# Optimization experiments

Measured on AMD Instinct MI355X. Metric: run time of the kernel, lower is better.

Reference implementation:

```python
import jax, jax.numpy as jnp
import numpy as np

PATCH = 16
H_RES, W_RES = 512, 512
PREFIX = 8
NUM_HEADS = 12
DIM = 768
GAUSS_STD = 5.0


def gauss_addition():
    # n_patches = (w//16, h//16); addition[(i,j),(k,l)] = exp(-((i-k)^2+(j-l)^2)/(2*std^2))
    d1, d2 = W_RES // PATCH, H_RES // PATCH  # (32, 32)
    inv2s2 = 1.0 / (2.0 * GAUSS_STD * GAUSS_STD)
    i = jnp.arange(d1, dtype=jnp.float32)
    j = jnp.arange(d2, dtype=jnp.float32)
    Ai = jnp.exp(-((i[:, None] - i[None, :]) ** 2) * inv2s2)  # [d1,d1]
    Aj = jnp.exp(-((j[:, None] - j[None, :]) ** 2) * inv2s2)  # [d2,d2]
    add = jnp.einsum('ik,jl->ijkl', Ai, Aj).reshape(d1 * d2, d1 * d2)
    # zero rows/cols for the prefix tokens (prepended)
    return jnp.pad(add, ((PREFIX, 0), (PREFIX, 0)))  # [N,N]


def setup_inputs() -> dict:
    key = jax.random.key(0)
    ks = jax.random.split(key, 5)
    N = (W_RES // PATCH) * (H_RES // PATCH) + PREFIX  # 1032
    B, C = 8, DIM
    x = jax.random.normal(ks[0], (B, N, C), dtype=jnp.float32)
    w_qkv = jax.random.normal(ks[1], (3 * C, C), dtype=jnp.float32) * 0.02
    b_qkv = jax.random.normal(ks[2], (3 * C,), dtype=jnp.float32) * 0.02
    w_proj = jax.random.normal(ks[3], (C, C), dtype=jnp.float32) * 0.02
    b_proj = jax.random.normal(ks[4], (C,), dtype=jnp.float32) * 0.02
    return {'x': x, 'w_qkv': w_qkv, 'b_qkv': b_qkv, 'w_proj': w_proj, 'b_proj': b_proj}


def reference(x, w_qkv, b_qkv, w_proj, b_proj):
    B, N, C = x.shape
    H = NUM_HEADS
    hd = C // H
    scale = hd ** -0.5
    qkv = x @ w_qkv.T + b_qkv              # [B,N,3C]
    k = qkv[..., C:2 * C].reshape(B, N, H, hd)
    v = qkv[..., 2 * C:].reshape(B, N, H, hd)
    add = gauss_addition().astype(x.dtype)  # [N,N], broadcast over B,H
    scores = jnp.einsum('bnhd,bmhd->bhnm', k, k) * scale + add
    attn = jax.nn.softmax(scores, axis=-1)
    out = jnp.einsum('bhnm,bmhd->bnhd', attn, v).reshape(B, N, C)
    return out @ w_proj.T + b_proj
```

## Files before the change

### kernel.cpp

```cpp
#include <hip/hip_runtime.h>
#include <hip/hip_bf16.h>

typedef unsigned short u16;
typedef __bf16 bf16x8 __attribute__((ext_vector_type(8)));
typedef __bf16 bf16x4 __attribute__((ext_vector_type(4)));
typedef float f32x4 __attribute__((ext_vector_type(4)));

#define DEVI __device__ __forceinline__

#if __has_builtin(__builtin_amdgcn_exp2f)
#define EXP2 __builtin_amdgcn_exp2f
#else
#define EXP2 exp2f
#endif

constexpr int Bn = 8, Nn = 1032, Cn = 768, Hn = 12, HDn = 64;
constexpr int NQPc = 1088;
constexpr int NVM = 1088;
constexpr int MTOT = Bn * Nn;
constexpr int MPAD = 8320;
constexpr int KVN = 1536;
constexpr int PFXc = 8;
constexpr int NPADQ = NVM - Nn;
constexpr float SCALEc = 0.125f;
constexpr float LOG2Ec = 1.4426950408889634f;
constexpr float C1c = SCALEc * LOG2Ec;
constexpr float INV2S2c = 0.02f;
constexpr float K2c = INV2S2c * LOG2Ec;

constexpr size_t OFF_XB  = 0;
constexpr size_t SZ_XB   = (size_t)MPAD * Cn * 2;
constexpr size_t OFF_AT  = OFF_XB;
constexpr size_t OFF_WKV = OFF_XB + SZ_XB;
constexpr size_t SZ_WKV  = (size_t)KVN * Cn * 2;
constexpr size_t OFF_WP  = OFF_WKV + SZ_WKV;
constexpr size_t SZ_WP   = (size_t)Cn * Cn * 2;
constexpr size_t OFF_K   = OFF_WP + SZ_WP;
constexpr size_t SZ_K    = (size_t)Bn * Hn * NQPc * HDn * 2;
constexpr size_t OFF_V   = OFF_K + SZ_K;
constexpr size_t SZ_V    = (size_t)Bn * Hn * HDn * NVM * 2;

DEVI u16 f2bf(float f) {
  __bf16 h = (__bf16)f;
  return *reinterpret_cast<u16*>(&h);
}

DEVI void glds16(const void* g, void* l) {
  __builtin_amdgcn_global_load_lds((const __attribute__((address_space(1))) void*)g,
                                   (__attribute__((address_space(3))) void*)l, 16, 0, 0);
}

__global__ __launch_bounds__(256) void prep_kernel(
    const float* __restrict__ x, const float* __restrict__ wqkv,
    const float* __restrict__ wproj, u16* __restrict__ xb,
    u16* __restrict__ wkvb, u16* __restrict__ wpb,
    u16* __restrict__ khead, u16* __restrict__ vT) {
  const int n1 = MPAD * Cn / 4, n2 = KVN * Cn / 4, n3 = Cn * Cn / 4;
  const int z1 = 96 * 448;
  const int z2 = 6144 * 7;
  const int nc = n1 + n2 + n3;
  const int tot = nc + z1 + z2;
  for (int i = blockIdx.x * blockDim.x + threadIdx.x; i < tot; i += gridDim.x * blockDim.x) {
    if (i < nc) {
      const float* src; u16* dst;
      if (i < n1) {
        int e = i * 4;
        src = (e < MTOT * Cn) ? (x + e) : nullptr;
        dst = xb + e;
      } else if (i < n1 + n2) {
        int e = (i - n1) * 4;
        src = wqkv + Cn * Cn + e;
        dst = wkvb + e;
      } else {
        int e = (i - n1 - n2) * 4;
        src = wproj + e;
        dst = wpb + e;
      }
      float4 f = src ? *(const float4*)src : make_float4(0.f, 0.f, 0.f, 0.f);
      *(ushort4*)dst = make_ushort4(f2bf(f.x), f2bf(f.y), f2bf(f.z), f2bf(f.w));
    } else if (i < nc + z1) {
      int j = i - nc, bh = j / 448, c = j - bh * 448;
      char* dst = (char*)khead + ((size_t)bh * NQPc + Nn) * HDn * 2 + c * 16;
      *(ushort4*)dst = make_ushort4(0, 0, 0, 0);
      *(ushort4*)(dst + 8) = make_ushort4(0, 0, 0, 0);
    } else {
      int j = i - nc - z1, st = j / 7, c = j - st * 7;
      char* dst = (char*)vT + ((size_t)st * NVM + Nn) * 2 + c * 16;
      *(ushort4*)dst = make_ushort4(0, 0, 0, 0);
      *(ushort4*)(dst + 8) = make_ushort4(0, 0, 0, 0);
    }
  }
}

DEVI void gemm_mainloop(const u16* __restrict__ A, const u16* __restrict__ Bm,
                        int m0, int n0, char* sA, char* sB, f32x4 (&acc)[4][4]) {
  const int tid = threadIdx.x, lane = tid & 63, w = tid >> 6;
  const int ln = lane & 15, lg = lane >> 4;
  const int wm = (w >> 1) * 64, wn = (w & 1) * 64;
  for (int kt = 0; kt < 12; ++kt) {
#pragma unroll
    for (int i = 0; i < 4; ++i) {
      const int c = i * 256 + tid, r = c >> 3, cb = c & 7, gcb = cb ^ (r & 7);
      const char* ga = (const char*)(A + (size_t)(m0 + r) * Cn + kt * 64) + gcb * 16;
      glds16(ga, sA + i * 4096 + w * 1024);
      const char* gb = (const char*)(Bm + (size_t)(n0 + r) * Cn + kt * 64) + gcb * 16;
      glds16(gb, sB + i * 4096 + w * 1024);
    }
    __syncthreads();
#pragma unroll
    for (int ks = 0; ks < 2; ++ks) {
      bf16x8 af[4], bfr[4];
#pragma unroll
      for (int s = 0; s < 4; ++s) {
        const int ra = wm + s * 16 + ln;
        af[s] = *(const bf16x8*)(sA + ra * 128 + (((ks * 4 + lg) ^ (ra & 7)) << 4));
        const int rb = wn + s * 16 + ln;
        bfr[s] = *(const bf16x8*)(sB + rb * 128 + (((ks * 4 + lg) ^ (rb & 7)) << 4));
      }
#pragma unroll
      for (int s = 0; s < 4; ++s)
#pragma unroll
        for (int t = 0; t < 4; ++t)
          acc[s][t] = __builtin_amdgcn_mfma_f32_16x16x32_bf16(af[s], bfr[t], acc[s][t], 0, 0, 0);
    }
    __syncthreads();
  }
}

__global__ __launch_bounds__(256) void kv_gemm(
    const u16* __restrict__ xb, const u16* __restrict__ wkvb,
    const float* __restrict__ bqkv, u16* __restrict__ khead, u16* __restrict__ vT) {
  __shared__ __align__(16) char smem[34816];
  char* sA = smem;
  char* sB = smem + 16384;
  const int bid = blockIdx.x;
  const int xcd = bid & 7, loc = bid >> 3;
  const int wgid = (xcd < 4) ? xcd * 98 + loc : 392 + (xcd - 4) * 97 + loc;
  const int m0 = (wgid / 12) * 128, n0 = (wgid % 12) * 128;
  f32x4 acc[4][4] = {};
  gemm_mainloop(xb, wkvb, m0, n0, sA, sB, acc);
  const int tid = threadIdx.x, lane = tid & 63, w = tid >> 6;
  const int ln = lane & 15, lg = lane >> 4;
  const int wm = (w >> 1) * 64, wn = (w & 1) * 64;
  const bool isV = (n0 >= Cn);
  u16* T = (u16*)smem;
  __syncthreads();
  if (!isV) {
#pragma unroll
    for (int t = 0; t < 4; ++t) {
      const int c = wn + t * 16 + ln;
      const float bias = bqkv[Cn + n0 + c];
#pragma unroll
      for (int s = 0; s < 4; ++s)
#pragma unroll
        for (int r = 0; r < 4; ++r)
          T[(wm + s * 16 + lg * 4 + r) * 136 + c] = f2bf(acc[s][t][r] + bias);
    }
    __syncthreads();
    const int h0 = n0 >> 6;
#pragma unroll
    for (int i = 0; i < 8; ++i) {
      const int runid = w * 64 + i * 8 + (lane >> 3);
      const int mloc = runid >> 1, hh = runid & 1;
      const int m = m0 + mloc;
      if (m < MTOT) {
        const int b = m / Nn, nr = m - b * Nn;
        const int d0 = (lane & 7) * 8;
        *(uint4*)&khead[((size_t)(b * Hn + h0 + hh) * NQPc + nr) * HDn + d0] =
            *(const uint4*)&T[mloc * 136 + hh * 64 + d0];
      }
    }
  } else {
#pragma unroll
    for (int t = 0; t < 4; ++t) {
      const int c = wn + t * 16 + ln;
      const float bias = bqkv[Cn + n0 + c];
#pragma unroll
      for (int s = 0; s < 4; ++s)
#pragma unroll
        for (int r = 0; r < 4; ++r)
          T[c * 136 + wm + s * 16 + lg * 4 + r] = f2bf(acc[s][t][r] + bias);
    }
    __syncthreads();
    const int vch0 = n0 - Cn;
#pragma unroll
    for (int i = 0; i < 8; ++i) {
      const int c = w * 32 + i * 4 + lg;
      const int vch = vch0 + c, h = vch >> 6, d = vch & 63;
      const int m = m0 + ln * 8;
      if (m < MTOT) {
        const int b = m / Nn, nr = m - b * Nn;
        *(uint4*)&vT[((size_t)(b * Hn + h) * HDn + d) * NVM + nr] =
            *(const uint4*)&T[c * 136 + ln * 8];
      }
    }
  }
}

__global__ __launch_bounds__(256, 4) void attn_kernel(
    const u16* __restrict__ khead, const u16* __restrict__ vT, u16* __restrict__ attn) {
  __shared__ __align__(16) char sK[2][8192];
  __shared__ __align__(16) char sV[2][8192];
  __shared__ __align__(16) char sP[4][2048];
  const int tid = threadIdx.x, lane = tid & 63, w = tid >> 6;
  const int ln = lane & 15, lg = lane >> 4;
  const int bid = blockIdx.x;

  bf16x8 ones8;
#pragma unroll
  for (int i = 0; i < 8; ++i) ones8[i] = (__bf16)1.0f;

  if (bid < 768) {
    const int xcd = bid & 7, loc = bid >> 3;
    const int lid = xcd * 96 + loc;
    const int qt = lid & 7, bh = lid >> 3;
    const int qb = PFXc + qt * 128 + w * 32;

    bf16x8 qf[2][2];
#pragma unroll
    for (int qg = 0; qg < 2; ++qg) {
      const char* qp = (const char*)(khead + ((size_t)bh * NQPc + qb + qg * 16 + ln) * HDn);
#pragma unroll
      for (int kc = 0; kc < 2; ++kc)
        qf[qg][kc] = *(const bf16x8*)(qp + kc * 64 + lg * 16);
    }

    const float c2 = EXP2(-2.0f * K2c);
    float ajr[2][8];
    float a0[2], a1[2], a2[2], fr[2];
#pragma unroll
    for (int qg = 0; qg < 2; ++qg) {
      const int pq = qt * 128 + w * 32 + qg * 16 + ln;
      const int iq = pq >> 5, jq = pq & 31;
#pragma unroll
      for (int t = 0; t < 8; ++t) {
        const int jm = (lg * 4 - 8 + (t >> 2) * 16 + (t & 3)) & 31;
        const float d = (float)(jq - jm);
        ajr[qg][t] = EXP2(-d * d * K2c);
      }
      const float d1 = (float)(iq + 1), d0 = (float)iq, dm = (float)(iq - 1);
      a0[qg] = EXP2(-d1 * d1 * K2c) * LOG2Ec;
      a1[qg] = EXP2(-d0 * d0 * K2c) * LOG2Ec;
      a2[qg] = EXP2(-dm * dm * K2c) * LOG2Ec;
      fr[qg] = EXP2((2.0f * (float)iq - 3.0f) * K2c);
    }

    const char* ksrc = (const char*)(khead + (size_t)bh * NQPc * HDn);
    const char* vsrc = (const char*)(vT + (size_t)bh * HDn * NVM);

#define STAGE(buf, mb) do { \
  _Pragma("unroll") for (int i_ = 0; i_ < 2; ++i_) { \
    const int c_ = i_ * 256 + tid, r_ = c_ >> 3, gcb_ = (c_ & 7) ^ (r_ & 7); \
    glds16(ksrc + (size_t)((mb) + r_) * 128 + gcb_ * 16, sK[buf] + i_ * 4096 + w * 1024); \
    glds16(vsrc + (size_t)r_ * (NVM * 2) + (mb) * 2 + gcb_ * 16, sV[buf] + i_ * 4096 + w * 1024); \
  } } while (0)

    f32x4 oacc[4][2] = {};
    f32x4 dacc[2] = {};
    STAGE(0, 0);

    for (int mc = 0; mc < 17; ++mc) {
      const int cur = mc & 1;
      const int mb = mc * 64;
      if (mc < 16) {
        STAGE(cur ^ 1, mb + 64);
        asm volatile("s_waitcnt vmcnt(4)" ::: "memory");
      } else {
        asm volatile("s_waitcnt vmcnt(0)" ::: "memory");
      }
      __builtin_amdgcn_sched_barrier(0);
      __builtin_amdgcn_s_barrier();
      __builtin_amdgcn_sched_barrier(0);

      f32x4 sacc[4][2] = {};
      __builtin_amdgcn_s_setprio(1);
#pragma unroll
      for (int ms = 0; ms < 4; ++ms) {
        const int r = ms * 16 + ln;
#pragma unroll
        for (int kc = 0; kc < 2; ++kc) {
          bf16x8 kf = *(const bf16x8*)(sK[cur] + r * 128 + (((kc * 4 + lg) ^ (r & 7)) << 4));
          sacc[ms][0] = __builtin_amdgcn_mfma_f32_16x16x32_bf16(kf, qf[0][kc], sacc[ms][0], 0, 0, 0);
          sacc[ms][1] = __builtin_amdgcn_mfma_f32_16x16x32_bf16(kf, qf[1][kc], sacc[ms][1], 0, 0, 0);
        }
      }
      __builtin_amdgcn_s_setprio(0);

      bf16x8 pf[2][2];
#pragma unroll
      for (int qg = 0; qg < 2; ++qg) {
        const float b0 = (mc == 0) ? 0.f : a0[qg];
        const float b1 = (mc == 16) ? 0.f : a1[qg];
        const float b2 = (mc == 16) ? 0.f : a2[qg];
#pragma unroll
        for (int ms = 0; ms < 4; ++ms) {
          float al;
          if (ms == 0)      al = (lg < 2) ? b0 : b1;
          else if (ms == 1) al = b1;
          else if (ms == 2) al = (lg < 2) ? b1 : b2;
          else              al = b2;
          const int t0 = (ms & 1) * 4;
          const float p0 = EXP2(fmaf(sacc[ms][qg][0], C1c, al * ajr[qg][t0 + 0]));
          const float p1 = EXP2(fmaf(sacc[ms][qg][1], C1c, al * ajr[qg][t0 + 1]));
          const float p2 = EXP2(fmaf(sacc[ms][qg][2], C1c, al * ajr[qg][t0 + 2]));
          const float p3 = EXP2(fmaf(sacc[ms][qg][3], C1c, al * ajr[qg][t0 + 3]));
          bf16x4 pk;
          pk[0] = (__bf16)p0; pk[1] = (__bf16)p1; pk[2] = (__bf16)p2; pk[3] = (__bf16)p3;
          *(bf16x4*)(sP[w] + ln * 128 + ((ms * 32 + lg * 8) ^ ((ln & 7) << 4))) = pk;
        }
#pragma unroll
        for (int km = 0; km < 2; ++km)
          pf[qg][km] = *(const bf16x8*)(sP[w] + ln * 128 +
                                        ((km * 64 + lg * 16) ^ ((ln & 7) << 4)));
        a0[qg] = a2[qg];
        a1[qg] = a2[qg] * fr[qg]; fr[qg] *= c2;
        a2[qg] = a1[qg] * fr[qg]; fr[qg] *= c2;
      }

      __builtin_amdgcn_s_setprio(1);
      dacc[0] = __builtin_amdgcn_mfma_f32_16x16x32_bf16(pf[0][0], ones8, dacc[0], 0, 0, 0);
      dacc[0] = __builtin_amdgcn_mfma_f32_16x16x32_bf16(pf[0][1], ones8, dacc[0], 0, 0, 0);
      dacc[1] = __builtin_amdgcn_mfma_f32_16x16x32_bf16(pf[1][0], ones8, dacc[1], 0, 0, 0);
      dacc[1] = __builtin_amdgcn_mfma_f32_16x16x32_bf16(pf[1][1], ones8, dacc[1], 0, 0, 0);
#pragma unroll
      for (int ds = 0; ds < 4; ++ds) {
        const int r = ds * 16 + ln;
#pragma unroll
        for (int km = 0; km < 2; ++km) {
          bf16x8 vf = *(const bf16x8*)(sV[cur] + r * 128 + (((km * 4 + lg) ^ (r & 7)) << 4));
          oacc[ds][0] = __builtin_amdgcn_mfma_f32_16x16x32_bf16(pf[0][km], vf, oacc[ds][0], 0, 0, 0);
          oacc[ds][1] = __builtin_amdgcn_mfma_f32_16x16x32_bf16(pf[1][km], vf, oacc[ds][1], 0, 0, 0);
        }
      }
      __builtin_amdgcn_s_setprio(0);
      __builtin_amdgcn_sched_barrier(0);
      __builtin_amdgcn_s_barrier();
      __builtin_amdgcn_sched_barrier(0);
    }
#undef STAGE

    const int b = bh / Hn, h = bh - b * Hn;
#pragma unroll
    for (int qg = 0; qg < 2; ++qg) {
#pragma unroll
      for (int r = 0; r < 4; ++r) {
        const int qo = qb + qg * 16 + lg * 4 + r;
        const float dinv = 1.0f / (dacc[qg][r] - (float)NPADQ);
#pragma unroll
        for (int ds = 0; ds < 4; ++ds)
          attn[((size_t)(b * Nn + qo)) * Cn + h * HDn + ds * 16 + ln] =
              f2bf(oacc[ds][qg][r] * dinv);
      }
    }
  } else {
    const int bh = bid - 768;
    const char* ksrc = (const char*)(khead + (size_t)bh * NQPc * HDn);
    const char* vsrc = (const char*)(vT + (size_t)bh * HDn * NVM);
    const char* qp = (const char*)(khead + ((size_t)bh * NQPc + ln) * HDn);
    bf16x8 qf[2];
    qf[0] = *(const bf16x8*)(qp + lg * 16);
    qf[1] = *(const bf16x8*)(qp + 64 + lg * 16);

    f32x4 oacc[4] = {};
    f32x4 dacc = {};
    for (int mc = w; mc < 17; mc += 4) {
      const int mb = mc * 64;
      f32x4 sacc[4] = {};
#pragma unroll
      for (int ms = 0; ms < 4; ++ms) {
        const char* kp = ksrc + (size_t)(mb + ms * 16 + ln) * 128 + lg * 16;
        bf16x8 kf0 = *(const bf16x8*)(kp);
        bf16x8 kf1 = *(const bf16x8*)(kp + 64);
        sacc[ms] = __builtin_amdgcn_mfma_f32_16x16x32_bf16(kf0, qf[0], sacc[ms], 0, 0, 0);
        sacc[ms] = __builtin_amdgcn_mfma_f32_16x16x32_bf16(kf1, qf[1], sacc[ms], 0, 0, 0);
      }
#pragma unroll
      for (int ms = 0; ms < 4; ++ms) {
        bf16x4 pk;
        pk[0] = (__bf16)EXP2(sacc[ms][0] * C1c);
        pk[1] = (__bf16)EXP2(sacc[ms][1] * C1c);
        pk[2] = (__bf16)EXP2(sacc[ms][2] * C1c);
        pk[3] = (__bf16)EXP2(sacc[ms][3] * C1c);
        *(bf16x4*)(sP[w] + ln * 128 + ((ms * 32 + lg * 8) ^ ((ln & 7) << 4))) = pk;
      }
      bf16x8 pf[2];
#pragma unroll
      for (int km = 0; km < 2; ++km)
        pf[km] = *(const bf16x8*)(sP[w] + ln * 128 + ((km * 64 + lg * 16) ^ ((ln & 7) << 4)));
      dacc = __builtin_amdgcn_mfma_f32_16x16x32_bf16(pf[0], ones8, dacc, 0, 0, 0);
      dacc = __builtin_amdgcn_mfma_f32_16x16x32_bf16(pf[1], ones8, dacc, 0, 0, 0);
#pragma unroll
      for (int ds = 0; ds < 4; ++ds) {
        const char* vp = vsrc + (size_t)(ds * 16 + ln) * (NVM * 2) + mb * 2 + lg * 16;
#pragma unroll
        for (int km = 0; km < 2; ++km) {
          bf16x8 vf = *(const bf16x8*)(vp + km * 64);
          oacc[ds] = __builtin_amdgcn_mfma_f32_16x16x32_bf16(pf[km], vf, oacc[ds], 0, 0, 0);
        }
      }
    }
    char* sKf = (char*)sK;
    char* sVf = (char*)sV;
    __syncthreads();
#pragma unroll
    for (int ds = 0; ds < 4; ++ds)
      *(f32x4*)(sKf + (((w * 4 + ds) * 64 + lane) << 4)) = oacc[ds];
    *(f32x4*)(sVf + ((w * 64 + lane) << 4)) = dacc;
    __syncthreads();
    f32x4 osum = {}, dsum = {};
#pragma unroll
    for (int wp = 0; wp < 4; ++wp) {
      osum += *(const f32x4*)(sKf + (((wp * 4 + w) * 64 + lane) << 4));
      dsum += *(const f32x4*)(sVf + ((wp * 64 + lane) << 4));
    }
    const int b = bh / Hn, h = bh - b * Hn;
#pragma unroll
    for (int r = 0; r < 4; ++r) {
      const int q = lg * 4 + r;
      if (q < PFXc)
        attn[((size_t)(b * Nn + q)) * Cn + h * HDn + w * 16 + ln] =
            f2bf(osum[r] / (dsum[r] - (float)NPADQ));
    }
  }
}

__global__ __launch_bounds__(256) void proj_gemm(
    const u16* __restrict__ at, const u16* __restrict__ wpb,
    const float* __restrict__ bproj, float* __restrict__ out) {
  __shared__ __align__(16) char sA[16384];
  __shared__ __align__(16) char sB[16384];
  const int bid = blockIdx.x;
  const int xcd = bid & 7, loc = bid >> 3;
  const int wgid = (xcd < 6) ? xcd * 49 + loc : 294 + (xcd - 6) * 48 + loc;
  const int m0 = (wgid / 6) * 128, n0 = (wgid % 6) * 128;
  f32x4 acc[4][4] = {};
  gemm_mainloop(at, wpb, m0, n0, sA, sB, acc);
  const int tid = threadIdx.x, lane = tid & 63, w = tid >> 6;
  const int ln = lane & 15, lg = lane >> 4;
  const int wm = (w >> 1) * 64, wn = (w & 1) * 64;
#pragma unroll
  for (int t = 0; t < 4; ++t) {
    const int n = n0 + wn + t * 16 + ln;
    const float bias = bproj[n];
#pragma unroll
    for (int s = 0; s < 4; ++s) {
#pragma unroll
      for (int r = 0; r < 4; ++r) {
        const int m = m0 + wm + s * 16 + lg * 4 + r;
        if (m < MTOT) out[(size_t)m * Cn + n] = acc[s][t][r] + bias;
      }
    }
  }
}

extern "C" void kernel_launch(void* const* d_in, const int* in_sizes, int n_in,
                              void* d_out, int out_size, void* d_ws, size_t ws_size,
                              hipStream_t stream) {
  const float* x     = (const float*)d_in[0];
  const float* wqkv  = (const float*)d_in[1];
  const float* bqkv  = (const float*)d_in[2];
  const float* wproj = (const float*)d_in[3];
  const float* bproj = (const float*)d_in[4];
  char* ws = (char*)d_ws;
  u16* xb    = (u16*)(ws + OFF_XB);
  u16* wkvb  = (u16*)(ws + OFF_WKV);
  u16* wpb   = (u16*)(ws + OFF_WP);
  u16* khead = (u16*)(ws + OFF_K);
  u16* vT    = (u16*)(ws + OFF_V);
  u16* attn  = (u16*)(ws + OFF_AT);

  prep_kernel<<<2048, 256, 0, stream>>>(x, wqkv, wproj, xb, wkvb, wpb, khead, vT);
  kv_gemm<<<780, 256, 0, stream>>>(xb, wkvb, bqkv, khead, vT);
  attn_kernel<<<864, 256, 0, stream>>>(khead, vT, attn);
  proj_gemm<<<390, 256, 0, stream>>>(attn, wpb, bproj, (float*)d_out);
}
```

Before: 124.0 us.

## Load K/V fragments directly from global memory instead of LDS double-buffering

The attention kernel's main path drops the async global-to-LDS double-buffered staging of K and V tiles, along with the block barriers and priority hints. Each wave now reads K and V MFMA fragments straight from global memory through the cache, and shared memory shrinks to a single buffer that holds only the P scratch and the reduction area. The launch-bounds occupancy hint is removed, and prefix blocks remap their batch-head index across XCDs. This removes block-level synchronisation and LDS traffic, but it gives up explicit prefetch overlap and shared reuse of K/V across the four waves, so the path now relies on L1/L2 hits.

New measurement: 172.9 us. 1.39x slower.

```diff
diff --git a/kernel.cpp b/kernel.cpp
--- a/kernel.cpp
+++ b/kernel.cpp
@@ -197,14 +197,13 @@
   }
 }
 
-__global__ __launch_bounds__(256, 4) void attn_kernel(
+__global__ __launch_bounds__(256) void attn_kernel(
     const u16* __restrict__ khead, const u16* __restrict__ vT, u16* __restrict__ attn) {
-  __shared__ __align__(16) char sK[2][8192];
-  __shared__ __align__(16) char sV[2][8192];
-  __shared__ __align__(16) char sP[4][2048];
+  __shared__ __align__(16) char smem[20480];
   const int tid = threadIdx.x, lane = tid & 63, w = tid >> 6;
   const int ln = lane & 15, lg = lane >> 4;
   const int bid = blockIdx.x;
+  char* sPw = smem + w * 2048;
 
   bf16x8 ones8;
 #pragma unroll
@@ -248,43 +247,22 @@
     const char* ksrc = (const char*)(khead + (size_t)bh * NQPc * HDn);
     const char* vsrc = (const char*)(vT + (size_t)bh * HDn * NVM);
 
-#define STAGE(buf, mb) do { \
-  _Pragma("unroll") for (int i_ = 0; i_ < 2; ++i_) { \
-    const int c_ = i_ * 256 + tid, r_ = c_ >> 3, gcb_ = (c_ & 7) ^ (r_ & 7); \
-    glds16(ksrc + (size_t)((mb) + r_) * 128 + gcb_ * 16, sK[buf] + i_ * 4096 + w * 1024); \
-    glds16(vsrc + (size_t)r_ * (NVM * 2) + (mb) * 2 + gcb_ * 16, sV[buf] + i_ * 4096 + w * 1024); \
-  } } while (0)
-
     f32x4 oacc[4][2] = {};
     f32x4 dacc[2] = {};
-    STAGE(0, 0);
 
     for (int mc = 0; mc < 17; ++mc) {
-      const int cur = mc & 1;
       const int mb = mc * 64;
-      if (mc < 16) {
-        STAGE(cur ^ 1, mb + 64);
-        asm volatile("s_waitcnt vmcnt(4)" ::: "memory");
-      } else {
-        asm volatile("s_waitcnt vmcnt(0)" ::: "memory");
-      }
-      __builtin_amdgcn_sched_barrier(0);
-      __builtin_amdgcn_s_barrier();
-      __builtin_amdgcn_sched_barrier(0);
-
       f32x4 sacc[4][2] = {};
-      __builtin_amdgcn_s_setprio(1);
 #pragma unroll
       for (int ms = 0; ms < 4; ++ms) {
-        const int r = ms * 16 + ln;
-#pragma unroll
-        for (int kc = 0; kc < 2; ++kc) {
-          bf16x8 kf = *(const bf16x8*)(sK[cur] + r * 128 + (((kc * 4 + lg) ^ (r & 7)) << 4));
-          sacc[ms][0] = __builtin_amdgcn_mfma_f32_16x16x32_bf16(kf, qf[0][kc], sacc[ms][0], 0, 0, 0);
-          sacc[ms][1] = __builtin_amdgcn_mfma_f32_16x16x32_bf16(kf, qf[1][kc], sacc[ms][1], 0, 0, 0);
-        }
-      }
-      __builtin_amdgcn_s_setprio(0);
+        const char* kp = ksrc + (size_t)(mb + ms * 16 + ln) * 128 + lg * 16;
+        bf16x8 kf0 = *(const bf16x8*)(kp);
+        bf16x8 kf1 = *(const bf16x8*)(kp + 64);
+        sacc[ms][0] = __builtin_amdgcn_mfma_f32_16x16x32_bf16(kf0, qf[0][0], sacc[ms][0], 0, 0, 0);
+        sacc[ms][0] = __builtin_amdgcn_mfma_f32_16x16x32_bf16(kf1, qf[0][1], sacc[ms][0], 0, 0, 0);
+        sacc[ms][1] = __builtin_amdgcn_mfma_f32_16x16x32_bf16(kf0, qf[1][0], sacc[ms][1], 0, 0, 0);
+        sacc[ms][1] = __builtin_amdgcn_mfma_f32_16x16x32_bf16(kf1, qf[1][1], sacc[ms][1], 0, 0, 0);
+      }
 
       bf16x8 pf[2][2];
 #pragma unroll
@@ -306,38 +284,32 @@
           const float p3 = EXP2(fmaf(sacc[ms][qg][3], C1c, al * ajr[qg][t0 + 3]));
           bf16x4 pk;
           pk[0] = (__bf16)p0; pk[1] = (__bf16)p1; pk[2] = (__bf16)p2; pk[3] = (__bf16)p3;
-          *(bf16x4*)(sP[w] + ln * 128 + ((ms * 32 + lg * 8) ^ ((ln & 7) << 4))) = pk;
+          *(bf16x4*)(sPw + ln * 128 + ((ms * 32 + lg * 8) ^ ((ln & 7) << 4))) = pk;
         }
 #pragma unroll
         for (int km = 0; km < 2; ++km)
-          pf[qg][km] = *(const bf16x8*)(sP[w] + ln * 128 +
+          pf[qg][km] = *(const bf16x8*)(sPw + ln * 128 +
                                         ((km * 64 + lg * 16) ^ ((ln & 7) << 4)));
         a0[qg] = a2[qg];
         a1[qg] = a2[qg] * fr[qg]; fr[qg] *= c2;
         a2[qg] = a1[qg] * fr[qg]; fr[qg] *= c2;
       }
 
-      __builtin_amdgcn_s_setprio(1);
       dacc[0] = __builtin_amdgcn_mfma_f32_16x16x32_bf16(pf[0][0], ones8, dacc[0], 0, 0, 0);
       dacc[0] = __builtin_amdgcn_mfma_f32_16x16x32_bf16(pf[0][1], ones8, dacc[0], 0, 0, 0);
       dacc[1] = __builtin_amdgcn_mfma_f32_16x16x32_bf16(pf[1][0], ones8, dacc[1], 0, 0, 0);
       dacc[1] = __builtin_amdgcn_mfma_f32_16x16x32_bf16(pf[1][1], ones8, dacc[1], 0, 0, 0);
 #pragma unroll
       for (int ds = 0; ds < 4; ++ds) {
-        const int r = ds * 16 + ln;
+        const char* vp = vsrc + (size_t)(ds * 16 + ln) * (NVM * 2) + mb * 2 + lg * 16;
 #pragma unroll
         for (int km = 0; km < 2; ++km) {
-          bf16x8 vf = *(const bf16x8*)(sV[cur] + r * 128 + (((km * 4 + lg) ^ (r & 7)) << 4));
+          bf16x8 vf = *(const bf16x8*)(vp + km * 64);
           oacc[ds][0] = __builtin_amdgcn_mfma_f32_16x16x32_bf16(pf[0][km], vf, oacc[ds][0], 0, 0, 0);
           oacc[ds][1] = __builtin_amdgcn_mfma_f32_16x16x32_bf16(pf[1][km], vf, oacc[ds][1], 0, 0, 0);
         }
       }
-      __builtin_amdgcn_s_setprio(0);
-      __builtin_amdgcn_sched_barrier(0);
-      __builtin_amdgcn_s_barrier();
-      __builtin_amdgcn_sched_barrier(0);
-    }
-#undef STAGE
+    }
 
     const int b = bh / Hn, h = bh - b * Hn;
 #pragma unroll
@@ -353,7 +325,8 @@
       }
     }
   } else {
-    const int bh = bid - 768;
+    const int i = bid - 768;
+    const int bh = (i & 7) * 12 + (i >> 3);
     const char* ksrc = (const char*)(khead + (size_t)bh * NQPc * HDn);
     const char* vsrc = (const char*)(vT + (size_t)bh * HDn * NVM);
     const char* qp = (const char*)(khead + ((size_t)bh * NQPc + ln) * HDn);
@@ -381,12 +354,12 @@
         pk[1] = (__bf16)EXP2(sacc[ms][1] * C1c);
         pk[2] = (__bf16)EXP2(sacc[ms][2] * C1c);
         pk[3] = (__bf16)EXP2(sacc[ms][3] * C1c);
-        *(bf16x4*)(sP[w] + ln * 128 + ((ms * 32 + lg * 8) ^ ((ln & 7) << 4))) = pk;
+        *(bf16x4*)(sPw + ln * 128 + ((ms * 32 + lg * 8) ^ ((ln & 7) << 4))) = pk;
       }
       bf16x8 pf[2];
 #pragma unroll
       for (int km = 0; km < 2; ++km)
-        pf[km] = *(const bf16x8*)(sP[w] + ln * 128 + ((km * 64 + lg * 16) ^ ((ln & 7) << 4)));
+        pf[km] = *(const bf16x8*)(sPw + ln * 128 + ((km * 64 + lg * 16) ^ ((ln & 7) << 4)));
       dacc = __builtin_amdgcn_mfma_f32_16x16x32_bf16(pf[0], ones8, dacc, 0, 0, 0);
       dacc = __builtin_amdgcn_mfma_f32_16x16x32_bf16(pf[1], ones8, dacc, 0, 0, 0);
 #pragma unroll
@@ -399,8 +372,8 @@
         }
       }
     }
-    char* sKf = (char*)sK;
-    char* sVf = (char*)sV;
+    char* sKf = smem;
+    char* sVf = smem + 16384;
     __syncthreads();
 #pragma unroll
     for (int ds = 0; ds < 4; ++ds)
```
